# Kernel tuning notes

Hardware: AMD Instinct MI355X
Metric: run time of the kernel (lower is better)

## Reference

```python
import jax, jax.numpy as jnp
import numpy as np

N_NODES = 100000
N_EDGES = 3200000
N_FEATS = 512
HIDDEN = 16
N_CLASSES = 40


def gcn_conv(x, edge_index, W, b):
    """PyG-style GCNConv: linear -> symmetric-normalized scatter-add -> bias."""
    n = x.shape[0]
    src, dst = edge_index[0], edge_index[1]
    # add self-loops
    loop = jnp.arange(n, dtype=src.dtype)
    src = jnp.concatenate([src, loop])
    dst = jnp.concatenate([dst, loop])
    # symmetric normalization deg^{-1/2}[src] * deg^{-1/2}[dst]
    deg = jax.ops.segment_sum(jnp.ones_like(src, dtype=x.dtype), dst, num_segments=n)
    dinv = jnp.where(deg > 0, jax.lax.rsqrt(jnp.maximum(deg, 1.0)), 0.0)
    norm = dinv[src] * dinv[dst]  # [E+N]
    h = x @ W                     # [N, out]
    msg = h[src] * norm[:, None]  # gather + scale, [E+N, out]
    out = jax.ops.segment_sum(msg, dst, num_segments=n)  # scatter-add at targets
    return out + b


def setup_inputs() -> dict:
    key = jax.random.key(0)
    k1, k2, k3, k4 = jax.random.split(key, 4)
    x = jax.random.normal(k1, (N_NODES, N_FEATS), dtype=jnp.float32)
    edge_index = jax.random.randint(k2, (2, N_EDGES), 0, N_NODES, dtype=jnp.int64)
    # Glorot-ish scaled weights
    W1 = jax.random.normal(k3, (N_FEATS, HIDDEN), dtype=jnp.float32) * (1.0 / np.sqrt(N_FEATS))
    b1 = jnp.zeros((HIDDEN,), dtype=jnp.float32)
    W2 = jax.random.normal(k4, (HIDDEN, N_CLASSES), dtype=jnp.float32) * (1.0 / np.sqrt(HIDDEN))
    b2 = jnp.zeros((N_CLASSES,), dtype=jnp.float32)
    return {"x": x, "edge_index": edge_index, "W1": W1, "b1": b1, "W2": W2, "b2": b2}


def reference(x, edge_index, W1, b1, W2, b2):
    h = gcn_conv(x, edge_index, W1, b1)
    h = jax.nn.relu(h)
    # dropout is identity in eval mode
    h = gcn_conv(h, edge_index, W2, b2)
    return jax.nn.log_softmax(h, axis=1)
```

## Files before the change

kernel.cpp:

```cpp
#include <hip/hip_runtime.h>
#include <hip/hip_bf16.h>

#define NN 100000
#define NE 3200000
#define NF 512
#define NH 16
#define NC 40
#define NB 782
#define CAP 5120
#define NBLK 512
#define CHUNK 6250

typedef __attribute__((ext_vector_type(4))) float f32x4;
typedef __attribute__((ext_vector_type(8))) short bf16x8;

static __device__ __forceinline__ unsigned short f2b(float f) {
    unsigned int u = __float_as_uint(f);
    u += 0x7FFFu + ((u >> 16) & 1u);
    return (unsigned short)(u >> 16);
}


__global__ void __launch_bounds__(256) k_mshist(const int* __restrict__ ei,
                                                int* __restrict__ histG) {
    __shared__ int h[NB];
    for (int i = threadIdx.x; i < NB; i += 256) h[i] = 0;
    __syncthreads();
    int b = blockIdx.x;
    int e0 = b * CHUNK, e1 = min(NE, e0 + CHUNK);
    for (int e = e0 + threadIdx.x; e < e1; e += 256)
        atomicAdd(&h[((unsigned)ei[NE + e]) >> 7], 1);
    __syncthreads();
    for (int i = threadIdx.x; i < NB; i += 256)
        histG[b * NB + i] = h[i];
}


__global__ void __launch_bounds__(512) k_colscan(const int* __restrict__ histG,
                                                 int* __restrict__ ofsG,
                                                 int* __restrict__ bcnt) {
    __shared__ int sh[NBLK];
    int k = blockIdx.x;
    int t = threadIdx.x;
    int v = histG[t * NB + k];
    sh[t] = v;
    __syncthreads();
    for (int off = 1; off < NBLK; off <<= 1) {
        int add = (t >= off) ? sh[t - off] : 0;
        __syncthreads();
        sh[t] += add;
        __syncthreads();
    }
    ofsG[k * NBLK + t] = sh[t] - v;
    if (t == NBLK - 1) bcnt[k] = sh[t];
}


__global__ void k_bscan(const int* __restrict__ bcnt, int* __restrict__ bptr,
                        int* __restrict__ rowptr) {
    __shared__ int sh[1024];
    int t = threadIdx.x;
    int v = (t < NB) ? bcnt[t] : 0;
    sh[t] = v;
    __syncthreads();
    for (int off = 1; off < 1024; off <<= 1) {
        int add = (t >= off) ? sh[t - off] : 0;
        __syncthreads();
        sh[t] += add;
        __syncthreads();
    }
    if (t < NB) bptr[t] = sh[t] - v;
    if (t == 0) { bptr[NB] = NE; rowptr[NN] = NE; }
}


__global__ void __launch_bounds__(256) k_msscatter(const int* __restrict__ ei,
                                                   const int* __restrict__ bptr,
                                                   const int* __restrict__ ofsG,
                                                   unsigned int* __restrict__ pairs) {
    __shared__ int lcur[NB];
    int b = blockIdx.x;
    for (int k = threadIdx.x; k < NB; k += 256)
        lcur[k] = bptr[k] + ofsG[k * NBLK + b];
    __syncthreads();
    int e0 = b * CHUNK, e1 = min(NE, e0 + CHUNK);
    for (int e = e0 + threadIdx.x; e < e1; e += 256) {
        unsigned int s = (unsigned int)ei[e];
        unsigned int d = (unsigned int)ei[NE + e];
        int pos = atomicAdd(&lcur[d >> 7], 1);
        pairs[pos] = s | ((d & 127u) << 17);
    }
}


__global__ void __launch_bounds__(256) k_bsort(const unsigned int* __restrict__ pairs,
                                               const int* __restrict__ bptr,
                                               int* __restrict__ rowptr,
                                               float* __restrict__ dinv,
                                               int* __restrict__ ssrc) {
    __shared__ unsigned int ein[CAP];
    __shared__ unsigned int srt[CAP];
    __shared__ int lcnt[128], lofs[128], lcur[128];
    int b = blockIdx.x;
    int s0 = bptr[b], s1 = bptr[b + 1];
    int n = s1 - s0;
    for (int i = threadIdx.x; i < n; i += 256) ein[i] = pairs[s0 + i];
    if (threadIdx.x < 128) lcnt[threadIdx.x] = 0;
    __syncthreads();
    for (int i = threadIdx.x; i < n; i += 256) atomicAdd(&lcnt[ein[i] >> 17], 1);
    __syncthreads();
    if (threadIdx.x < 128) lofs[threadIdx.x] = lcnt[threadIdx.x];
    __syncthreads();
    for (int off = 1; off < 128; off <<= 1) {
        int add = 0;
        if (threadIdx.x < 128 && threadIdx.x >= off) add = lofs[threadIdx.x - off];
        __syncthreads();
        if (threadIdx.x < 128) lofs[threadIdx.x] += add;
        __syncthreads();
    }
    if (threadIdx.x < 128) {
        int excl = lofs[threadIdx.x] - lcnt[threadIdx.x];
        lcur[threadIdx.x] = excl;
        int node = b * 128 + threadIdx.x;
        if (node < NN) {
            rowptr[node] = s0 + excl;
            dinv[node] = rsqrtf((float)(lcnt[threadIdx.x] + 1));
        }
    }
    __syncthreads();
    for (int i = threadIdx.x; i < n; i += 256) {
        unsigned int v = ein[i];
        int pos = atomicAdd(&lcur[v >> 17], 1);
        srt[pos] = v & 0x1FFFFu;
    }
    __syncthreads();
    for (int i = threadIdx.x; i < n; i += 256) ssrc[s0 + i] = (int)srt[i];
}


__global__ void k_packW1(const float* __restrict__ W1, unsigned short* __restrict__ pack) {
    int idx = blockIdx.x * 256 + threadIdx.x;
    int s = idx >> 9;
    int l = (idx >> 3) & 63;
    int e = idx & 7;
    int k = s * 32 + (l >> 4) * 8 + e;
    int col = l & 15;
    pack[idx] = f2b(W1[k * 16 + col]);
}


__global__ void __launch_bounds__(256) k_gemm1(const float* __restrict__ x,
                                               const unsigned short* __restrict__ wp,
                                               const float* __restrict__ dinv,
                                               float* __restrict__ hs1) {
    int wave = threadIdx.x >> 6;
    int l = threadIdx.x & 63;
    int m0 = blockIdx.x * 64 + wave * 16;
    if (m0 >= NN) return;
    int row = m0 + (l & 15);
    int krow = (l >> 4) * 8;
    const float* xr = x + (size_t)row * NF + krow;
    const unsigned short* wl = wp + l * 8;

    f32x4 acc = {0.f, 0.f, 0.f, 0.f};
#pragma unroll 4
    for (int s = 0; s < 16; ++s) {
        f32x4 xa = *(const f32x4*)(xr + s * 32);
        f32x4 xb = *(const f32x4*)(xr + s * 32 + 4);
        union { bf16x8 v; unsigned short u[8]; } a;
        a.u[0] = f2b(xa.x); a.u[1] = f2b(xa.y); a.u[2] = f2b(xa.z); a.u[3] = f2b(xa.w);
        a.u[4] = f2b(xb.x); a.u[5] = f2b(xb.y); a.u[6] = f2b(xb.z); a.u[7] = f2b(xb.w);
        bf16x8 b = *(const bf16x8*)(wl + s * 512);
        acc = __builtin_amdgcn_mfma_f32_16x16x32_bf16(a.v, b, acc, 0, 0, 0);
    }
#pragma unroll
    for (int r = 0; r < 4; ++r) {
        int orow = m0 + (l >> 4) * 4 + r;
        hs1[(size_t)orow * NH + (l & 15)] = acc[r] * dinv[orow];
    }
}


__global__ void __launch_bounds__(256) k_agg(const float* __restrict__ hs,
                                             const int* __restrict__ rowptr,
                                             const int* __restrict__ ssrc,
                                             const float* __restrict__ dinv,
                                             const float* __restrict__ bias,
                                             float* __restrict__ hout, int do_relu) {
    int l = threadIdx.x & 63;
    int node = blockIdx.x * 4 + (threadIdx.x >> 6);
    if (node >= NN) return;
    int j = l & 15;
    int ec = l >> 4;
    float di = dinv[node];
    int s = rowptr[node];
    int epos = rowptr[node + 1];
    float acc = (ec == 0) ? hs[(size_t)node * NH + j] : 0.0f;
#pragma unroll 4
    for (int e = s + ec; e < epos; e += 4) {
        int src = ssrc[e];
        acc += hs[(size_t)src * NH + j];
    }
    acc += __shfl_xor(acc, 16, 64);
    acc += __shfl_xor(acc, 32, 64);
    if (ec == 0) {
        float o = acc * di;
        if (do_relu) o = fmaxf(o + bias[j], 0.0f) * di;
        hout[(size_t)node * NH + j] = o;
    }
}


__global__ void __launch_bounds__(256) k_out(const float* __restrict__ z2,
                                             const float* __restrict__ W2,
                                             const float* __restrict__ b2,
                                             float* __restrict__ out) {
    __shared__ float w[NH * NC];
    __shared__ float bb[NC];
    for (int i = threadIdx.x; i < NH * NC; i += 256) w[i] = W2[i];
    if (threadIdx.x < NC) bb[threadIdx.x] = b2[threadIdx.x];
    __syncthreads();
    int node = blockIdx.x * 256 + threadIdx.x;
    if (node >= NN) return;
    float z[NH];
    const f32x4* zp = (const f32x4*)(z2 + (size_t)node * NH);
#pragma unroll
    for (int q = 0; q < 4; ++q) {
        f32x4 v = zp[q];
        z[q * 4 + 0] = v.x; z[q * 4 + 1] = v.y; z[q * 4 + 2] = v.z; z[q * 4 + 3] = v.w;
    }
    float logit[NC];
#pragma unroll
    for (int c = 0; c < NC; ++c) logit[c] = bb[c];
#pragma unroll
    for (int k = 0; k < NH; ++k) {
        float zv = z[k];
#pragma unroll
        for (int c = 0; c < NC; ++c) logit[c] += zv * w[k * NC + c];
    }
    float mx = logit[0];
#pragma unroll
    for (int c = 1; c < NC; ++c) mx = fmaxf(mx, logit[c]);
    float sum = 0.f;
#pragma unroll
    for (int c = 0; c < NC; ++c) sum += __expf(logit[c] - mx);
    float lse = mx + __logf(sum);
    float* op = out + (size_t)node * NC;
#pragma unroll
    for (int c = 0; c < NC; ++c) op[c] = logit[c] - lse;
}


extern "C" void kernel_launch(void* const* d_in, const int* in_sizes, int n_in,
                              void* d_out, int out_size, void* d_ws, size_t ws_size,
                              hipStream_t stream) {
    const float* x  = (const float*)d_in[0];
    const int*   ei = (const int*)d_in[1];
    const float* W1 = (const float*)d_in[2];
    const float* b1 = (const float*)d_in[3];
    const float* W2 = (const float*)d_in[4];
    const float* b2 = (const float*)d_in[5];
    float* out = (float*)d_out;

    char* ws = (char*)d_ws;
    size_t off = 0;
    auto alloc = [&](size_t bytes) -> void* {
        void* p = ws + off;
        off += (bytes + 255) & ~(size_t)255;
        return p;
    };
    int* histG      = (int*)alloc((size_t)NBLK * NB * 4);
    int* ofsG       = (int*)alloc((size_t)NB * NBLK * 4);
    int* bcnt       = (int*)alloc((size_t)NB * 4);
    int* bptr       = (int*)alloc((size_t)(NB + 1) * 4);
    int* rowptr     = (int*)alloc((size_t)(NN + 1) * 4);
    float* dinv     = (float*)alloc((size_t)NN * 4);
    unsigned short* w1p = (unsigned short*)alloc(16 * 64 * 8 * 2);
    unsigned int* pairs = (unsigned int*)alloc((size_t)NE * 4);
    int* ssrc       = (int*)alloc((size_t)NE * 4);
    float* h1       = (float*)alloc((size_t)NN * NH * 4);
    float* r1       = (float*)alloc((size_t)NN * NH * 4);

    int nb = (NN + 255) / 256;

    k_packW1<<<32, 256, 0, stream>>>(W1, w1p);
    k_mshist<<<NBLK, 256, 0, stream>>>(ei, histG);
    k_colscan<<<NB, NBLK, 0, stream>>>(histG, ofsG, bcnt);
    k_bscan<<<1, 1024, 0, stream>>>(bcnt, bptr, rowptr);
    k_msscatter<<<NBLK, 256, 0, stream>>>(ei, bptr, ofsG, pairs);
    k_bsort<<<NB, 256, 0, stream>>>(pairs, bptr, rowptr, dinv, ssrc);
    k_gemm1<<<(NN + 63) / 64, 256, 0, stream>>>(x, w1p, dinv, h1);
    k_agg<<<NN / 4, 256, 0, stream>>>(h1, rowptr, ssrc, dinv, b1, r1, 1);
    k_agg<<<NN / 4, 256, 0, stream>>>(r1, rowptr, ssrc, dinv, nullptr, h1, 0);
    k_out<<<nb, 256, 0, stream>>>(h1, W2, b2, out);
}
```

Baseline: 251.3 us.

## Aggregate per 128-node bucket with LDS atomics, drop full CSR sort, bf16 features

Replaces the per-bucket counting sort that built a full CSR with a degree-only pass. Aggregation now works directly on bucketed (src, local dst) pairs, accumulating into shared memory with atomics per 128-node bucket. Hidden features are stored in bf16 to halve gather traffic, and the output projection plus log-softmax is fused into the second aggregation kernel. This removes the sort, the ssrc buffer and the separate output kernel. In exchange it adds LDS atomic contention, uses only 782 blocks, and loses precision from bf16 rounding.

```diff
diff --git a/kernel.cpp b/kernel.cpp
--- a/kernel.cpp
+++ b/kernel.cpp
@@ -7,7 +7,6 @@
 #define NH 16
 #define NC 40
 #define NB 782
-#define CAP 5120
 #define NBLK 512
 #define CHUNK 6250
 
@@ -18,6 +17,9 @@
     unsigned int u = __float_as_uint(f);
     u += 0x7FFFu + ((u >> 16) & 1u);
     return (unsigned short)(u >> 16);
+}
+static __device__ __forceinline__ float b2f(unsigned short u) {
+    return __uint_as_float(((unsigned int)u) << 16);
 }
 
 
@@ -56,8 +58,7 @@
 }
 
 
-__global__ void k_bscan(const int* __restrict__ bcnt, int* __restrict__ bptr,
-                        int* __restrict__ rowptr) {
+__global__ void k_bscan(const int* __restrict__ bcnt, int* __restrict__ bptr) {
     __shared__ int sh[1024];
     int t = threadIdx.x;
     int v = (t < NB) ? bcnt[t] : 0;
@@ -70,7 +71,7 @@
         __syncthreads();
     }
     if (t < NB) bptr[t] = sh[t] - v;
-    if (t == 0) { bptr[NB] = NE; rowptr[NN] = NE; }
+    if (t == 0) bptr[NB] = NE;
 }
 
 
@@ -93,48 +94,20 @@
 }
 
 
-__global__ void __launch_bounds__(256) k_bsort(const unsigned int* __restrict__ pairs,
-                                               const int* __restrict__ bptr,
-                                               int* __restrict__ rowptr,
-                                               float* __restrict__ dinv,
-                                               int* __restrict__ ssrc) {
-    __shared__ unsigned int ein[CAP];
-    __shared__ unsigned int srt[CAP];
-    __shared__ int lcnt[128], lofs[128], lcur[128];
-    int b = blockIdx.x;
+__global__ void __launch_bounds__(256) k_degb(const unsigned int* __restrict__ pairs,
+                                              const int* __restrict__ bptr,
+                                              float* __restrict__ dinv) {
+    __shared__ int lcnt[128];
+    int b = blockIdx.x;
+    if (threadIdx.x < 128) lcnt[threadIdx.x] = 0;
+    __syncthreads();
     int s0 = bptr[b], s1 = bptr[b + 1];
-    int n = s1 - s0;
-    for (int i = threadIdx.x; i < n; i += 256) ein[i] = pairs[s0 + i];
-    if (threadIdx.x < 128) lcnt[threadIdx.x] = 0;
-    __syncthreads();
-    for (int i = threadIdx.x; i < n; i += 256) atomicAdd(&lcnt[ein[i] >> 17], 1);
-    __syncthreads();
-    if (threadIdx.x < 128) lofs[threadIdx.x] = lcnt[threadIdx.x];
-    __syncthreads();
-    for (int off = 1; off < 128; off <<= 1) {
-        int add = 0;
-        if (threadIdx.x < 128 && threadIdx.x >= off) add = lofs[threadIdx.x - off];
-        __syncthreads();
-        if (threadIdx.x < 128) lofs[threadIdx.x] += add;
-        __syncthreads();
-    }
-    if (threadIdx.x < 128) {
-        int excl = lofs[threadIdx.x] - lcnt[threadIdx.x];
-        lcur[threadIdx.x] = excl;
-        int node = b * 128 + threadIdx.x;
-        if (node < NN) {
-            rowptr[node] = s0 + excl;
-            dinv[node] = rsqrtf((float)(lcnt[threadIdx.x] + 1));
-        }
-    }
-    __syncthreads();
-    for (int i = threadIdx.x; i < n; i += 256) {
-        unsigned int v = ein[i];
-        int pos = atomicAdd(&lcur[v >> 17], 1);
-        srt[pos] = v & 0x1FFFFu;
-    }
-    __syncthreads();
-    for (int i = threadIdx.x; i < n; i += 256) ssrc[s0 + i] = (int)srt[i];
+    for (int e = s0 + threadIdx.x; e < s1; e += 256)
+        atomicAdd(&lcnt[pairs[e] >> 17], 1);
+    __syncthreads();
+    int node = b * 128 + threadIdx.x;
+    if (threadIdx.x < 128 && node < NN)
+        dinv[node] = rsqrtf((float)(lcnt[threadIdx.x] + 1));
 }
 
 
@@ -152,7 +125,7 @@
 __global__ void __launch_bounds__(256) k_gemm1(const float* __restrict__ x,
                                                const unsigned short* __restrict__ wp,
                                                const float* __restrict__ dinv,
-                                               float* __restrict__ hs1) {
+                                               unsigned short* __restrict__ hs1) {
     int wave = threadIdx.x >> 6;
     int l = threadIdx.x & 63;
     int m0 = blockIdx.x * 64 + wave * 16;
@@ -176,78 +149,116 @@
 #pragma unroll
     for (int r = 0; r < 4; ++r) {
         int orow = m0 + (l >> 4) * 4 + r;
-        hs1[(size_t)orow * NH + (l & 15)] = acc[r] * dinv[orow];
-    }
-}
-
-
-__global__ void __launch_bounds__(256) k_agg(const float* __restrict__ hs,
-                                             const int* __restrict__ rowptr,
-                                             const int* __restrict__ ssrc,
-                                             const float* __restrict__ dinv,
-                                             const float* __restrict__ bias,
-                                             float* __restrict__ hout, int do_relu) {
-    int l = threadIdx.x & 63;
-    int node = blockIdx.x * 4 + (threadIdx.x >> 6);
-    if (node >= NN) return;
-    int j = l & 15;
-    int ec = l >> 4;
-    float di = dinv[node];
-    int s = rowptr[node];
-    int epos = rowptr[node + 1];
-    float acc = (ec == 0) ? hs[(size_t)node * NH + j] : 0.0f;
+        hs1[(size_t)orow * NH + (l & 15)] = f2b(acc[r] * dinv[orow]);
+    }
+}
+
+
+__global__ void __launch_bounds__(256) k_aggb1(const unsigned int* __restrict__ pairs,
+                                               const int* __restrict__ bptr,
+                                               const unsigned short* __restrict__ hs,
+                                               const float* __restrict__ dinv,
+                                               const float* __restrict__ b1,
+                                               unsigned short* __restrict__ r1) {
+    __shared__ float acc[128 * NH];
+    __shared__ float sh_di[128];
+    __shared__ float sh_b[NH];
+    int b = blockIdx.x;
+    int node0 = b * 128;
+    int t = threadIdx.x;
+    if (t < 128) sh_di[t] = (node0 + t < NN) ? dinv[node0 + t] : 0.0f;
+    if (t < NH) sh_b[t] = b1[t];
+    for (int i = t; i < 128 * NH; i += 256) {
+        int node = node0 + (i >> 4);
+        acc[i] = (node < NN) ? b2f(hs[(size_t)node * NH + (i & 15)]) : 0.0f;
+    }
+    __syncthreads();
+    int s0 = bptr[b], s1 = bptr[b + 1];
+    int j = t & 15;
+    int ec = t >> 4;
 #pragma unroll 4
-    for (int e = s + ec; e < epos; e += 4) {
-        int src = ssrc[e];
-        acc += hs[(size_t)src * NH + j];
-    }
-    acc += __shfl_xor(acc, 16, 64);
-    acc += __shfl_xor(acc, 32, 64);
-    if (ec == 0) {
-        float o = acc * di;
-        if (do_relu) o = fmaxf(o + bias[j], 0.0f) * di;
-        hout[(size_t)node * NH + j] = o;
-    }
-}
-
-
-__global__ void __launch_bounds__(256) k_out(const float* __restrict__ z2,
-                                             const float* __restrict__ W2,
-                                             const float* __restrict__ b2,
-                                             float* __restrict__ out) {
+    for (int e = s0 + ec; e < s1; e += 16) {
+        unsigned int v = pairs[e];
+        int src = v & 0x1FFFFu;
+        int ld = v >> 17;
+        atomicAdd(&acc[ld * NH + j], b2f(hs[(size_t)src * NH + j]));
+    }
+    __syncthreads();
+    for (int i = t; i < 128 * NH; i += 256) {
+        int n = i >> 4;
+        int node = node0 + n;
+        if (node < NN) {
+            float di = sh_di[n];
+            float v = fmaxf(acc[i] * di + sh_b[i & 15], 0.0f) * di;
+            r1[(size_t)node * NH + (i & 15)] = f2b(v);
+        }
+    }
+}
+
+
+__global__ void __launch_bounds__(256) k_aggb2(const unsigned int* __restrict__ pairs,
+                                               const int* __restrict__ bptr,
+                                               const unsigned short* __restrict__ rs,
+                                               const float* __restrict__ dinv,
+                                               const float* __restrict__ W2,
+                                               const float* __restrict__ b2,
+                                               float* __restrict__ out) {
+    __shared__ float acc[128 * NH];
+    __shared__ float sh_di[128];
     __shared__ float w[NH * NC];
     __shared__ float bb[NC];
-    for (int i = threadIdx.x; i < NH * NC; i += 256) w[i] = W2[i];
-    if (threadIdx.x < NC) bb[threadIdx.x] = b2[threadIdx.x];
-    __syncthreads();
-    int node = blockIdx.x * 256 + threadIdx.x;
-    if (node >= NN) return;
-    float z[NH];
-    const f32x4* zp = (const f32x4*)(z2 + (size_t)node * NH);
-#pragma unroll
-    for (int q = 0; q < 4; ++q) {
-        f32x4 v = zp[q];
-        z[q * 4 + 0] = v.x; z[q * 4 + 1] = v.y; z[q * 4 + 2] = v.z; z[q * 4 + 3] = v.w;
-    }
-    float logit[NC];
-#pragma unroll
-    for (int c = 0; c < NC; ++c) logit[c] = bb[c];
-#pragma unroll
-    for (int k = 0; k < NH; ++k) {
-        float zv = z[k];
-#pragma unroll
-        for (int c = 0; c < NC; ++c) logit[c] += zv * w[k * NC + c];
-    }
-    float mx = logit[0];
-#pragma unroll
-    for (int c = 1; c < NC; ++c) mx = fmaxf(mx, logit[c]);
-    float sum = 0.f;
-#pragma unroll
-    for (int c = 0; c < NC; ++c) sum += __expf(logit[c] - mx);
-    float lse = mx + __logf(sum);
-    float* op = out + (size_t)node * NC;
-#pragma unroll
-    for (int c = 0; c < NC; ++c) op[c] = logit[c] - lse;
+    int b = blockIdx.x;
+    int node0 = b * 128;
+    int t = threadIdx.x;
+    if (t < 128) sh_di[t] = (node0 + t < NN) ? dinv[node0 + t] : 0.0f;
+    for (int i = t; i < NH * NC; i += 256) w[i] = W2[i];
+    if (t < NC) bb[t] = b2[t];
+    for (int i = t; i < 128 * NH; i += 256) {
+        int node = node0 + (i >> 4);
+        acc[i] = (node < NN) ? b2f(rs[(size_t)node * NH + (i & 15)]) : 0.0f;
+    }
+    __syncthreads();
+    int s0 = bptr[b], s1 = bptr[b + 1];
+    int j = t & 15;
+    int ec = t >> 4;
+#pragma unroll 4
+    for (int e = s0 + ec; e < s1; e += 16) {
+        unsigned int v = pairs[e];
+        int src = v & 0x1FFFFu;
+        int ld = v >> 17;
+        atomicAdd(&acc[ld * NH + j], b2f(rs[(size_t)src * NH + j]));
+    }
+    __syncthreads();
+    int n = t >> 1;
+    int half = t & 1;
+    int node = node0 + n;
+    if (node < NN) {
+        float di = sh_di[n];
+        float z[NH];
+#pragma unroll
+        for (int k = 0; k < NH; ++k) z[k] = acc[n * NH + k] * di;
+        float lg[20];
+#pragma unroll
+        for (int c0 = 0; c0 < 20; ++c0) {
+            int c = half * 20 + c0;
+            float s = bb[c];
+#pragma unroll
+            for (int k = 0; k < NH; ++k) s += z[k] * w[k * NC + c];
+            lg[c0] = s;
+        }
+        float mx = lg[0];
+#pragma unroll
+        for (int c0 = 1; c0 < 20; ++c0) mx = fmaxf(mx, lg[c0]);
+        mx = fmaxf(mx, __shfl_xor(mx, 1, 64));
+        float sum = 0.f;
+#pragma unroll
+        for (int c0 = 0; c0 < 20; ++c0) sum += __expf(lg[c0] - mx);
+        sum += __shfl_xor(sum, 1, 64);
+        float lse = mx + __logf(sum);
+        float* op = out + (size_t)node * NC + half * 20;
+#pragma unroll
+        for (int c0 = 0; c0 < 20; ++c0) op[c0] = lg[c0] - lse;
+    }
 }
 
 
@@ -273,24 +284,19 @@
     int* ofsG       = (int*)alloc((size_t)NB * NBLK * 4);
     int* bcnt       = (int*)alloc((size_t)NB * 4);
     int* bptr       = (int*)alloc((size_t)(NB + 1) * 4);
-    int* rowptr     = (int*)alloc((size_t)(NN + 1) * 4);
     float* dinv     = (float*)alloc((size_t)NN * 4);
     unsigned short* w1p = (unsigned short*)alloc(16 * 64 * 8 * 2);
     unsigned int* pairs = (unsigned int*)alloc((size_t)NE * 4);
-    int* ssrc       = (int*)alloc((size_t)NE * 4);
-    float* h1       = (float*)alloc((size_t)NN * NH * 4);
-    float* r1       = (float*)alloc((size_t)NN * NH * 4);
-
-    int nb = (NN + 255) / 256;
+    unsigned short* h1  = (unsigned short*)alloc((size_t)NN * NH * 2);
+    unsigned short* r1  = (unsigned short*)alloc((size_t)NN * NH * 2);
 
     k_packW1<<<32, 256, 0, stream>>>(W1, w1p);
     k_mshist<<<NBLK, 256, 0, stream>>>(ei, histG);
     k_colscan<<<NB, NBLK, 0, stream>>>(histG, ofsG, bcnt);
-    k_bscan<<<1, 1024, 0, stream>>>(bcnt, bptr, rowptr);
+    k_bscan<<<1, 1024, 0, stream>>>(bcnt, bptr);
     k_msscatter<<<NBLK, 256, 0, stream>>>(ei, bptr, ofsG, pairs);
-    k_bsort<<<NB, 256, 0, stream>>>(pairs, bptr, rowptr, dinv, ssrc);
+    k_degb<<<NB, 256, 0, stream>>>(pairs, bptr, dinv);
     k_gemm1<<<(NN + 63) / 64, 256, 0, stream>>>(x, w1p, dinv, h1);
-    k_agg<<<NN / 4, 256, 0, stream>>>(h1, rowptr, ssrc, dinv, b1, r1, 1);
-    k_agg<<<NN / 4, 256, 0, stream>>>(r1, rowptr, ssrc, dinv, nullptr, h1, 0);
-    k_out<<<nb, 256, 0, stream>>>(h1, W2, b2, out);
-}
+    k_aggb1<<<NB, 256, 0, stream>>>(pairs, bptr, h1, dinv, b1, r1);
+    k_aggb2<<<NB, 256, 0, stream>>>(pairs, bptr, r1, dinv, W2, b2, out);
+}
```

Result: slower. 802.0 us (+219.1%).

## Store hidden features in bf16 and fuse layer-2 linear+log_softmax into aggregation

Applied to the files above, without the earlier changes.

Intermediate node features h1 and r1 are now stored as bf16 instead of fp32, which halves the bytes moved by the random gathers in both aggregation passes. The second aggregation kernel now also applies W2, the bias and log_softmax within each wave using shuffles, so the separate output kernel and its read of the fp32 intermediate are removed. In exchange, bf16 rounding of the hidden features lowers precision, and every aggregation block now loads W2 into shared memory and runs a full-wave reduction per node.

```diff
diff --git a/kernel.cpp b/kernel.cpp
--- a/kernel.cpp
+++ b/kernel.cpp
@@ -18,6 +18,9 @@
     unsigned int u = __float_as_uint(f);
     u += 0x7FFFu + ((u >> 16) & 1u);
     return (unsigned short)(u >> 16);
+}
+static __device__ __forceinline__ float b2f(unsigned short u) {
+    return __uint_as_float(((unsigned int)u) << 16);
 }
 
 
@@ -152,7 +155,7 @@
 __global__ void __launch_bounds__(256) k_gemm1(const float* __restrict__ x,
                                                const unsigned short* __restrict__ wp,
                                                const float* __restrict__ dinv,
-                                               float* __restrict__ hs1) {
+                                               unsigned short* __restrict__ hs1) {
     int wave = threadIdx.x >> 6;
     int l = threadIdx.x & 63;
     int m0 = blockIdx.x * 64 + wave * 16;
@@ -176,78 +179,82 @@
 #pragma unroll
     for (int r = 0; r < 4; ++r) {
         int orow = m0 + (l >> 4) * 4 + r;
-        hs1[(size_t)orow * NH + (l & 15)] = acc[r] * dinv[orow];
-    }
-}
-
-
-__global__ void __launch_bounds__(256) k_agg(const float* __restrict__ hs,
-                                             const int* __restrict__ rowptr,
-                                             const int* __restrict__ ssrc,
-                                             const float* __restrict__ dinv,
-                                             const float* __restrict__ bias,
-                                             float* __restrict__ hout, int do_relu) {
+        hs1[(size_t)orow * NH + (l & 15)] = f2b(acc[r] * dinv[orow]);
+    }
+}
+
+
+__global__ void __launch_bounds__(256) k_agg1(const unsigned short* __restrict__ hs,
+                                              const int* __restrict__ rowptr,
+                                              const int* __restrict__ ssrc,
+                                              const float* __restrict__ dinv,
+                                              const float* __restrict__ b1,
+                                              unsigned short* __restrict__ r1) {
     int l = threadIdx.x & 63;
     int node = blockIdx.x * 4 + (threadIdx.x >> 6);
-    if (node >= NN) return;
     int j = l & 15;
     int ec = l >> 4;
     float di = dinv[node];
     int s = rowptr[node];
-    int epos = rowptr[node + 1];
-    float acc = (ec == 0) ? hs[(size_t)node * NH + j] : 0.0f;
+    int e1 = rowptr[node + 1];
+    float acc = (ec == 0) ? b2f(hs[(size_t)node * NH + j]) : 0.0f;
 #pragma unroll 4
-    for (int e = s + ec; e < epos; e += 4) {
+    for (int e = s + ec; e < e1; e += 4) {
         int src = ssrc[e];
-        acc += hs[(size_t)src * NH + j];
+        acc += b2f(hs[(size_t)src * NH + j]);
     }
     acc += __shfl_xor(acc, 16, 64);
     acc += __shfl_xor(acc, 32, 64);
     if (ec == 0) {
-        float o = acc * di;
-        if (do_relu) o = fmaxf(o + bias[j], 0.0f) * di;
-        hout[(size_t)node * NH + j] = o;
-    }
-}
-
-
-__global__ void __launch_bounds__(256) k_out(const float* __restrict__ z2,
-                                             const float* __restrict__ W2,
-                                             const float* __restrict__ b2,
-                                             float* __restrict__ out) {
+        float o = fmaxf(acc * di + b1[j], 0.0f) * di;
+        r1[(size_t)node * NH + j] = f2b(o);
+    }
+}
+
+
+__global__ void __launch_bounds__(256) k_agg2(const unsigned short* __restrict__ rs,
+                                              const int* __restrict__ rowptr,
+                                              const int* __restrict__ ssrc,
+                                              const float* __restrict__ dinv,
+                                              const float* __restrict__ W2,
+                                              const float* __restrict__ b2,
+                                              float* __restrict__ out) {
     __shared__ float w[NH * NC];
     __shared__ float bb[NC];
-    for (int i = threadIdx.x; i < NH * NC; i += 256) w[i] = W2[i];
-    if (threadIdx.x < NC) bb[threadIdx.x] = b2[threadIdx.x];
-    __syncthreads();
-    int node = blockIdx.x * 256 + threadIdx.x;
-    if (node >= NN) return;
-    float z[NH];
-    const f32x4* zp = (const f32x4*)(z2 + (size_t)node * NH);
-#pragma unroll
-    for (int q = 0; q < 4; ++q) {
-        f32x4 v = zp[q];
-        z[q * 4 + 0] = v.x; z[q * 4 + 1] = v.y; z[q * 4 + 2] = v.z; z[q * 4 + 3] = v.w;
-    }
-    float logit[NC];
-#pragma unroll
-    for (int c = 0; c < NC; ++c) logit[c] = bb[c];
+    int t = threadIdx.x;
+    for (int i = t; i < NH * NC; i += 256) w[i] = W2[i];
+    if (t < NC) bb[t] = b2[t];
+    __syncthreads();
+    int l = t & 63;
+    int node = blockIdx.x * 4 + (t >> 6);
+    int j = l & 15;
+    int ec = l >> 4;
+    float di = dinv[node];
+    int s = rowptr[node];
+    int e1 = rowptr[node + 1];
+    float acc = (ec == 0) ? b2f(rs[(size_t)node * NH + j]) : 0.0f;
+#pragma unroll 4
+    for (int e = s + ec; e < e1; e += 4) {
+        int src = ssrc[e];
+        acc += b2f(rs[(size_t)src * NH + j]);
+    }
+    acc += __shfl_xor(acc, 16, 64);
+    acc += __shfl_xor(acc, 32, 64);
+    float zv = acc * di;
+    float lg = (l < NC) ? bb[l] : -1e30f;
 #pragma unroll
     for (int k = 0; k < NH; ++k) {
-        float zv = z[k];
+        float zk = __shfl(zv, k, 64);
+        if (l < NC) lg += zk * w[k * NC + l];
+    }
+    float mx = lg;
 #pragma unroll
-        for (int c = 0; c < NC; ++c) logit[c] += zv * w[k * NC + c];
-    }
-    float mx = logit[0];
+    for (int off = 1; off < 64; off <<= 1) mx = fmaxf(mx, __shfl_xor(mx, off, 64));
+    float ex = (l < NC) ? __expf(lg - mx) : 0.0f;
+    float sm = ex;
 #pragma unroll
-    for (int c = 1; c < NC; ++c) mx = fmaxf(mx, logit[c]);
-    float sum = 0.f;
-#pragma unroll
-    for (int c = 0; c < NC; ++c) sum += __expf(logit[c] - mx);
-    float lse = mx + __logf(sum);
-    float* op = out + (size_t)node * NC;
-#pragma unroll
-    for (int c = 0; c < NC; ++c) op[c] = logit[c] - lse;
+    for (int off = 1; off < 64; off <<= 1) sm += __shfl_xor(sm, off, 64);
+    if (l < NC) out[(size_t)node * NC + l] = lg - mx - __logf(sm);
 }
 
 
@@ -278,10 +285,8 @@
     unsigned short* w1p = (unsigned short*)alloc(16 * 64 * 8 * 2);
     unsigned int* pairs = (unsigned int*)alloc((size_t)NE * 4);
     int* ssrc       = (int*)alloc((size_t)NE * 4);
-    float* h1       = (float*)alloc((size_t)NN * NH * 4);
-    float* r1       = (float*)alloc((size_t)NN * NH * 4);
-
-    int nb = (NN + 255) / 256;
+    unsigned short* h1  = (unsigned short*)alloc((size_t)NN * NH * 2);
+    unsigned short* r1  = (unsigned short*)alloc((size_t)NN * NH * 2);
 
     k_packW1<<<32, 256, 0, stream>>>(W1, w1p);
     k_mshist<<<NBLK, 256, 0, stream>>>(ei, histG);
@@ -290,7 +295,6 @@
     k_msscatter<<<NBLK, 256, 0, stream>>>(ei, bptr, ofsG, pairs);
     k_bsort<<<NB, 256, 0, stream>>>(pairs, bptr, rowptr, dinv, ssrc);
     k_gemm1<<<(NN + 63) / 64, 256, 0, stream>>>(x, w1p, dinv, h1);
-    k_agg<<<NN / 4, 256, 0, stream>>>(h1, rowptr, ssrc, dinv, b1, r1, 1);
-    k_agg<<<NN / 4, 256, 0, stream>>>(r1, rowptr, ssrc, dinv, nullptr, h1, 0);
-    k_out<<<nb, 256, 0, stream>>>(h1, W2, b2, out);
-}
+    k_agg1<<<NN / 4, 256, 0, stream>>>(h1, rowptr, ssrc, dinv, b1, r1);
+    k_agg2<<<NN / 4, 256, 0, stream>>>(r1, rowptr, ssrc, dinv, W2, b2, out);
+}
```

New measurement: 248.5 us. Within noise of the previous version (-1.1%).
